# Performance work log

Measured on AMD Instinct MI355X. Metric: run time of the kernel, lower is better.

Reference implementation:

```python
import jax, jax.numpy as jnp
import numpy as np

OUT, IN, BLK, RANK = 4096, 4096, 32, 16
N_BLOCKS = IN // BLK  # 128
Q_ZERO = 128.0  # center of unsigned code range, maps codes to signed values


def setup_inputs() -> dict:
    key = jax.random.key(0)
    ks = jax.random.split(key, 6)
    x = jax.random.normal(ks[0], (4, 2048, IN), dtype=jnp.float32)
    # GGML-style block-quantized weight: int codes in blocks of 32 + per-block fp scale
    q_weight = jax.random.randint(ks[1], (OUT, N_BLOCKS, BLK), 0, 256, dtype=jnp.int32)
    scales = jax.random.uniform(ks[2], (OUT, N_BLOCKS), dtype=jnp.float32) * 0.02
    # LoRA patch applied to dequantized weight
    lora_up = jax.random.normal(ks[3], (OUT, RANK), dtype=jnp.float32) * 0.02
    lora_down = jax.random.normal(ks[4], (RANK, IN), dtype=jnp.float32) * 0.02
    bias = jax.random.normal(ks[5], (OUT,), dtype=jnp.float32)
    return {"x": x, "q_weight": q_weight, "scales": scales,
            "lora_up": lora_up, "lora_down": lora_down, "bias": bias}


def reference(x, q_weight, scales, lora_up, lora_down, bias):
    # 1) dequantize: per-block scale * centered int codes -> full fp weight [OUT, IN]
    w = (q_weight.astype(jnp.float32) - Q_ZERO) * scales[:, :, None]
    w = w.reshape(OUT, IN)
    # 2) apply LoRA patch to the dequantized weight (patch function in get_weight)
    w = w + lora_up @ lora_down
    # 3) delegate to the linear forward operation: y = x @ W^T + b
    return jnp.einsum('bsd,od->bso', x, w) + bias
```

## Files before the change

kernel.cpp:

```cpp
#include <hip/hip_runtime.h>
#include <cstdint>
#include <cstddef>

#define M_TOT 8192
#define N_TOT 4096
#define K_TOT 4096
#define RANK  16

#define BM 256
#define BN 256
#define BK 64
#define NT (K_TOT / BK)

typedef float f32x4 __attribute__((ext_vector_type(4)));
typedef __bf16 bf16x8 __attribute__((ext_vector_type(8)));
typedef unsigned short u16x8 __attribute__((ext_vector_type(8)));

__device__ __forceinline__ unsigned short f32_to_bf16(float f) {
    union { float f; uint32_t u; } v; v.f = f;
    uint32_t r = v.u + (0x7fffu + ((v.u >> 16) & 1u));
    return (unsigned short)(r >> 16);
}

__device__ __forceinline__ void gload_lds16(const void* g, void* l) {
    __builtin_amdgcn_global_load_lds(
        (const __attribute__((address_space(1))) void*)g,
        (__attribute__((address_space(3))) void*)l,
        16, 0, 0);
}

__global__ __launch_bounds__(256) void convert_x_kernel(const float* __restrict__ x,
                                                        unsigned short* __restrict__ xb,
                                                        int n8) {
    int i = blockIdx.x * 256 + threadIdx.x;
    if (i >= n8) return;
    float4 a = ((const float4*)x)[2 * (size_t)i];
    float4 b = ((const float4*)x)[2 * (size_t)i + 1];
    u16x8 o;
    o[0] = f32_to_bf16(a.x); o[1] = f32_to_bf16(a.y);
    o[2] = f32_to_bf16(a.z); o[3] = f32_to_bf16(a.w);
    o[4] = f32_to_bf16(b.x); o[5] = f32_to_bf16(b.y);
    o[6] = f32_to_bf16(b.z); o[7] = f32_to_bf16(b.w);
    *(u16x8*)&xb[(size_t)i * 8] = o;
}

__global__ __launch_bounds__(256) void build_w_kernel(const int* __restrict__ q,
                                                      const float* __restrict__ scales,
                                                      const float* __restrict__ up,
                                                      const float* __restrict__ down,
                                                      unsigned short* __restrict__ W) {
    const int o0 = blockIdx.x * 4;
    const int t = threadIdx.x;
    __shared__ float u[4][RANK];
    if (t < 64) u[t >> 4][t & 15] = up[(o0 + (t >> 4)) * RANK + (t & 15)];
    __syncthreads();

#pragma unroll
    for (int cc = 0; cc < 2; cc++) {
        const int c = t + 256 * cc;
        const int k0 = c * 8;
        float acc[4][8];
#pragma unroll
        for (int row = 0; row < 4; row++) {
            const int o = o0 + row;
            int4 qa = *(const int4*)&q[(size_t)o * K_TOT + k0];
            int4 qb = *(const int4*)&q[(size_t)o * K_TOT + k0 + 4];
            const float s = scales[o * (K_TOT / 32) + (k0 >> 5)];
            acc[row][0] = (float)(qa.x - 128) * s;
            acc[row][1] = (float)(qa.y - 128) * s;
            acc[row][2] = (float)(qa.z - 128) * s;
            acc[row][3] = (float)(qa.w - 128) * s;
            acc[row][4] = (float)(qb.x - 128) * s;
            acc[row][5] = (float)(qb.y - 128) * s;
            acc[row][6] = (float)(qb.z - 128) * s;
            acc[row][7] = (float)(qb.w - 128) * s;
        }
#pragma unroll
        for (int r = 0; r < RANK; r++) {
            float4 da = *(const float4*)&down[r * K_TOT + k0];
            float4 db = *(const float4*)&down[r * K_TOT + k0 + 4];
#pragma unroll
            for (int row = 0; row < 4; row++) {
                const float ur = u[row][r];
                acc[row][0] += ur * da.x; acc[row][1] += ur * da.y;
                acc[row][2] += ur * da.z; acc[row][3] += ur * da.w;
                acc[row][4] += ur * db.x; acc[row][5] += ur * db.y;
                acc[row][6] += ur * db.z; acc[row][7] += ur * db.w;
            }
        }
#pragma unroll
        for (int row = 0; row < 4; row++) {
            u16x8 o8;
#pragma unroll
            for (int j = 0; j < 8; j++) o8[j] = f32_to_bf16(acc[row][j]);
            *(u16x8*)&W[(size_t)(o0 + row) * K_TOT + k0] = o8;
        }
    }
}

#define BARRIER() do { asm volatile("" ::: "memory"); \
                       __builtin_amdgcn_s_barrier(); \
                       asm volatile("" ::: "memory"); } while (0)
#define WAITL0()  asm volatile("s_waitcnt lgkmcnt(0)" ::: "memory")
#define SCHED0()  __builtin_amdgcn_sched_barrier(0)

__global__ __launch_bounds__(512, 2) void gemm_bt_kernel(const unsigned short* __restrict__ A,
                                                         const unsigned short* __restrict__ B,
                                                         const float* __restrict__ bias,
                                                         float* __restrict__ C) {
    __shared__ unsigned short As[2][2][128 * BK];
    __shared__ unsigned short Bs[2][2][128 * BK];

    const int tid  = (int)threadIdx.x;
    const int wave = tid >> 6;
    const int lane = tid & 63;
    const int wm   = wave >> 2;
    const int wn   = wave & 3;
    const int wbh  = wn >> 1;
    const int wbr  = (wn & 1) * 64;

    int lin = (int)(blockIdx.y * gridDim.x + blockIdx.x);
    lin = (lin & 7) * 64 + (lin >> 3);
    const int tile_n = (lin & 15) * BN;
    const int tile_m = (lin >> 4) * BM;

    const int srow  = tid >> 3;
    const int sk    = ((tid & 7) ^ (srow & 7)) * 8;
    const int wbase = wave * 512;

    const int l16  = lane & 15;
    const int quad = lane >> 4;
    const int sw   = l16 & 7;
    const int slot0 = ((quad ^ sw) * 8);
    const int slot1 = (((4 + quad) ^ sw) * 8);

    const unsigned short* aBase = A + (size_t)(tile_m + srow) * K_TOT + sk;
    const unsigned short* bBase = B + (size_t)(tile_n + srow) * K_TOT + sk;

#define STAGE_A(d, h, t) do { \
    gload_lds16(aBase + (size_t)((h) * 128) * K_TOT + (size_t)(t) * BK, &As[d][h][wbase]); \
    gload_lds16(aBase + (size_t)((h) * 128 + 64) * K_TOT + (size_t)(t) * BK, &As[d][h][4096 + wbase]); \
  } while (0)
#define STAGE_B(d, h, t) do { \
    gload_lds16(bBase + (size_t)((h) * 128) * K_TOT + (size_t)(t) * BK, &Bs[d][h][wbase]); \
    gload_lds16(bBase + (size_t)((h) * 128 + 64) * K_TOT + (size_t)(t) * BK, &Bs[d][h][4096 + wbase]); \
  } while (0)

    f32x4 acc[8][4];
#pragma unroll
    for (int i = 0; i < 8; i++)
#pragma unroll
        for (int j = 0; j < 4; j++) { f32x4 z = {0.f, 0.f, 0.f, 0.f}; acc[i][j] = z; }

    STAGE_A(0, 0, 0); STAGE_A(0, 1, 0);
    STAGE_B(0, 0, 0); STAGE_B(0, 1, 0);
    STAGE_A(1, 0, 1); STAGE_A(1, 1, 1);
    asm volatile("s_waitcnt vmcnt(4)" ::: "memory");
    BARRIER();

    for (int t = 0; t < NT; ++t) {
        const int cur = t & 1, nxt = cur ^ 1;
        const unsigned short* __restrict__ Ah = &As[cur][wm][l16 * BK];
        const unsigned short* __restrict__ Bh = &Bs[cur][wbh][(wbr + l16) * BK];

        bf16x8 bA[4], bB[4], aF[4];

        if (t + 1 < NT) STAGE_B(nxt, 0, t + 1);
#pragma unroll
        for (int ni = 0; ni < 4; ni++) bA[ni] = *(const bf16x8*)&Bh[(ni * 16) * BK + slot0];
#pragma unroll
        for (int mi = 0; mi < 4; mi++) aF[mi] = *(const bf16x8*)&Ah[(mi * 16) * BK + slot0];
        BARRIER();
        WAITL0();
        SCHED0();
        __builtin_amdgcn_s_setprio(1);
#pragma unroll
        for (int mi = 0; mi < 4; mi++)
#pragma unroll
            for (int ni = 0; ni < 4; ni++)
                acc[mi][ni] = __builtin_amdgcn_mfma_f32_16x16x32_bf16(aF[mi], bA[ni], acc[mi][ni], 0, 0, 0);
        __builtin_amdgcn_s_setprio(0);
        SCHED0();
        BARRIER();

        if (t + 1 < NT) STAGE_B(nxt, 1, t + 1);
#pragma unroll
        for (int ni = 0; ni < 4; ni++) bB[ni] = *(const bf16x8*)&Bh[(ni * 16) * BK + slot1];
#pragma unroll
        for (int mi = 0; mi < 4; mi++) aF[mi] = *(const bf16x8*)&Ah[(mi * 16) * BK + slot1];
        BARRIER();
        WAITL0();
        SCHED0();
        __builtin_amdgcn_s_setprio(1);
#pragma unroll
        for (int mi = 0; mi < 4; mi++)
#pragma unroll
            for (int ni = 0; ni < 4; ni++)
                acc[mi][ni] = __builtin_amdgcn_mfma_f32_16x16x32_bf16(aF[mi], bB[ni], acc[mi][ni], 0, 0, 0);
        __builtin_amdgcn_s_setprio(0);
        SCHED0();
        BARRIER();

#pragma unroll
        for (int mi = 0; mi < 4; mi++) aF[mi] = *(const bf16x8*)&Ah[((mi + 4) * 16) * BK + slot0];
        BARRIER();
        WAITL0();
        SCHED0();
        __builtin_amdgcn_s_setprio(1);
#pragma unroll
        for (int mi = 0; mi < 4; mi++)
#pragma unroll
            for (int ni = 0; ni < 4; ni++)
                acc[mi + 4][ni] = __builtin_amdgcn_mfma_f32_16x16x32_bf16(aF[mi], bA[ni], acc[mi + 4][ni], 0, 0, 0);
        __builtin_amdgcn_s_setprio(0);
        SCHED0();
        BARRIER();

#pragma unroll
        for (int mi = 0; mi < 4; mi++) aF[mi] = *(const bf16x8*)&Ah[((mi + 4) * 16) * BK + slot1];
        BARRIER();
        if (t + 2 < NT) { STAGE_A(cur, 0, t + 2); STAGE_A(cur, 1, t + 2); }
        WAITL0();
        SCHED0();
        __builtin_amdgcn_s_setprio(1);
#pragma unroll
        for (int mi = 0; mi < 4; mi++)
#pragma unroll
            for (int ni = 0; ni < 4; ni++)
                acc[mi + 4][ni] = __builtin_amdgcn_mfma_f32_16x16x32_bf16(aF[mi], bB[ni], acc[mi + 4][ni], 0, 0, 0);
        __builtin_amdgcn_s_setprio(0);
        SCHED0();
        if (t + 1 < NT) {
            if (t + 2 < NT) asm volatile("s_waitcnt vmcnt(4)" ::: "memory");
            else            asm volatile("s_waitcnt vmcnt(0)" ::: "memory");
        }
        BARRIER();
    }

#pragma unroll
    for (int ni = 0; ni < 4; ni++) {
        const int col = tile_n + wn * 64 + ni * 16 + l16;
        const float bv = bias[col];
#pragma unroll
        for (int mi = 0; mi < 8; mi++) {
#pragma unroll
            for (int r = 0; r < 4; r++) {
                const int row = tile_m + wm * 128 + mi * 16 + quad * 4 + r;
                C[(size_t)row * N_TOT + col] = acc[mi][ni][r] + bv;
            }
        }
    }
#undef STAGE_A
#undef STAGE_B
}

extern "C" void kernel_launch(void* const* d_in, const int* in_sizes, int n_in,
                              void* d_out, int out_size, void* d_ws, size_t ws_size,
                              hipStream_t stream) {
    const float* x      = (const float*)d_in[0];
    const int*   q      = (const int*)d_in[1];
    const float* scales = (const float*)d_in[2];
    const float* up     = (const float*)d_in[3];
    const float* down   = (const float*)d_in[4];
    const float* bias   = (const float*)d_in[5];
    float* out = (float*)d_out;

    unsigned short* xb = (unsigned short*)d_ws;
    unsigned short* wb = xb + (size_t)M_TOT * K_TOT;

    const int n8 = M_TOT * K_TOT / 8;
    convert_x_kernel<<<n8 / 256, 256, 0, stream>>>(x, xb, n8);
    build_w_kernel<<<N_TOT / 4, 256, 0, stream>>>(q, scales, up, down, wb);
    gemm_bt_kernel<<<dim3(N_TOT / BN, M_TOT / BM), 512, 0, stream>>>(xb, wb, bias, out);
}
```

Measured before the change: 598.0 us.

## Restructure GEMM main loop with inline-asm LDS reads and one-tile-ahead A prefetch

The main loop of the bf16 GEMM now loads its LDS fragments through inline-asm ds_read_b128 on precomputed LDS addresses, and the global-to-LDS loads are issued after those reads. The A prefetch moves from two tiles ahead into the current buffer to one tile ahead into the next buffer, and every iteration ends with a full vmcnt(0) wait. The aim is cheaper address math and a simpler, more regular schedule. The cost is a shallower prefetch for A and a full drain of outstanding global loads each iteration, which can expose memory latency.

```diff
diff --git a/kernel.cpp b/kernel.cpp
--- a/kernel.cpp
+++ b/kernel.cpp
@@ -27,6 +27,16 @@
         (const __attribute__((address_space(1))) void*)g,
         (__attribute__((address_space(3))) void*)l,
         16, 0, 0);
+}
+
+__device__ __forceinline__ unsigned lds_addr(const void* p) {
+    return (unsigned)(uintptr_t)(const __attribute__((address_space(3))) void*)p;
+}
+
+__device__ __forceinline__ bf16x8 dsr(unsigned addr) {
+    bf16x8 r;
+    asm volatile("ds_read_b128 %0, %1" : "=v"(r) : "v"(addr));
+    return r;
 }
 
 __global__ __launch_bounds__(256) void convert_x_kernel(const float* __restrict__ x,
@@ -102,6 +112,7 @@
                        __builtin_amdgcn_s_barrier(); \
                        asm volatile("" ::: "memory"); } while (0)
 #define WAITL0()  asm volatile("s_waitcnt lgkmcnt(0)" ::: "memory")
+#define VMCNT0()  asm volatile("s_waitcnt vmcnt(0)" ::: "memory")
 #define SCHED0()  __builtin_amdgcn_sched_barrier(0)
 
 __global__ __launch_bounds__(512, 2) void gemm_bt_kernel(const unsigned short* __restrict__ A,
@@ -154,86 +165,85 @@
 
     STAGE_A(0, 0, 0); STAGE_A(0, 1, 0);
     STAGE_B(0, 0, 0); STAGE_B(0, 1, 0);
-    STAGE_A(1, 0, 1); STAGE_A(1, 1, 1);
-    asm volatile("s_waitcnt vmcnt(4)" ::: "memory");
+    VMCNT0();
     BARRIER();
 
     for (int t = 0; t < NT; ++t) {
         const int cur = t & 1, nxt = cur ^ 1;
-        const unsigned short* __restrict__ Ah = &As[cur][wm][l16 * BK];
-        const unsigned short* __restrict__ Bh = &Bs[cur][wbh][(wbr + l16) * BK];
-
-        bf16x8 bA[4], bB[4], aF[4];
-
+
+        const unsigned AhB = lds_addr(&As[cur][wm][l16 * BK]);
+        const unsigned BhB = lds_addr(&Bs[cur][wbh][(wbr + l16) * BK]);
+        const unsigned a0 = AhB + slot0 * 2, a1 = AhB + slot1 * 2;
+        const unsigned b0 = BhB + slot0 * 2, b1 = BhB + slot1 * 2;
+
+        bf16x8 bA[4], bB[4], aK[4];
+
+#pragma unroll
+        for (int ni = 0; ni < 4; ni++) bA[ni] = dsr(b0 + ni * 2048);
+#pragma unroll
+        for (int mi = 0; mi < 4; mi++) aK[mi] = dsr(a0 + mi * 2048);
         if (t + 1 < NT) STAGE_B(nxt, 0, t + 1);
-#pragma unroll
-        for (int ni = 0; ni < 4; ni++) bA[ni] = *(const bf16x8*)&Bh[(ni * 16) * BK + slot0];
-#pragma unroll
-        for (int mi = 0; mi < 4; mi++) aF[mi] = *(const bf16x8*)&Ah[(mi * 16) * BK + slot0];
-        BARRIER();
-        WAITL0();
-        SCHED0();
-        __builtin_amdgcn_s_setprio(1);
-#pragma unroll
-        for (int mi = 0; mi < 4; mi++)
-#pragma unroll
-            for (int ni = 0; ni < 4; ni++)
-                acc[mi][ni] = __builtin_amdgcn_mfma_f32_16x16x32_bf16(aF[mi], bA[ni], acc[mi][ni], 0, 0, 0);
-        __builtin_amdgcn_s_setprio(0);
-        SCHED0();
-        BARRIER();
-
+        BARRIER();
+        WAITL0();
+        SCHED0();
+        __builtin_amdgcn_s_setprio(1);
+#pragma unroll
+        for (int mi = 0; mi < 4; mi++)
+#pragma unroll
+            for (int ni = 0; ni < 4; ni++)
+                acc[mi][ni] = __builtin_amdgcn_mfma_f32_16x16x32_bf16(aK[mi], bA[ni], acc[mi][ni], 0, 0, 0);
+        __builtin_amdgcn_s_setprio(0);
+        SCHED0();
+        BARRIER();
+
+#pragma unroll
+        for (int ni = 0; ni < 4; ni++) bB[ni] = dsr(b1 + ni * 2048);
+#pragma unroll
+        for (int mi = 0; mi < 4; mi++) aK[mi] = dsr(a1 + mi * 2048);
         if (t + 1 < NT) STAGE_B(nxt, 1, t + 1);
-#pragma unroll
-        for (int ni = 0; ni < 4; ni++) bB[ni] = *(const bf16x8*)&Bh[(ni * 16) * BK + slot1];
-#pragma unroll
-        for (int mi = 0; mi < 4; mi++) aF[mi] = *(const bf16x8*)&Ah[(mi * 16) * BK + slot1];
-        BARRIER();
-        WAITL0();
-        SCHED0();
-        __builtin_amdgcn_s_setprio(1);
-#pragma unroll
-        for (int mi = 0; mi < 4; mi++)
-#pragma unroll
-            for (int ni = 0; ni < 4; ni++)
-                acc[mi][ni] = __builtin_amdgcn_mfma_f32_16x16x32_bf16(aF[mi], bB[ni], acc[mi][ni], 0, 0, 0);
-        __builtin_amdgcn_s_setprio(0);
-        SCHED0();
-        BARRIER();
-
-#pragma unroll
-        for (int mi = 0; mi < 4; mi++) aF[mi] = *(const bf16x8*)&Ah[((mi + 4) * 16) * BK + slot0];
-        BARRIER();
-        WAITL0();
-        SCHED0();
-        __builtin_amdgcn_s_setprio(1);
-#pragma unroll
-        for (int mi = 0; mi < 4; mi++)
-#pragma unroll
-            for (int ni = 0; ni < 4; ni++)
-                acc[mi + 4][ni] = __builtin_amdgcn_mfma_f32_16x16x32_bf16(aF[mi], bA[ni], acc[mi + 4][ni], 0, 0, 0);
-        __builtin_amdgcn_s_setprio(0);
-        SCHED0();
-        BARRIER();
-
-#pragma unroll
-        for (int mi = 0; mi < 4; mi++) aF[mi] = *(const bf16x8*)&Ah[((mi + 4) * 16) * BK + slot1];
-        BARRIER();
-        if (t + 2 < NT) { STAGE_A(cur, 0, t + 2); STAGE_A(cur, 1, t + 2); }
-        WAITL0();
-        SCHED0();
-        __builtin_amdgcn_s_setprio(1);
-#pragma unroll
-        for (int mi = 0; mi < 4; mi++)
-#pragma unroll
-            for (int ni = 0; ni < 4; ni++)
-                acc[mi + 4][ni] = __builtin_amdgcn_mfma_f32_16x16x32_bf16(aF[mi], bB[ni], acc[mi + 4][ni], 0, 0, 0);
-        __builtin_amdgcn_s_setprio(0);
-        SCHED0();
-        if (t + 1 < NT) {
-            if (t + 2 < NT) asm volatile("s_waitcnt vmcnt(4)" ::: "memory");
-            else            asm volatile("s_waitcnt vmcnt(0)" ::: "memory");
-        }
+        BARRIER();
+        WAITL0();
+        SCHED0();
+        __builtin_amdgcn_s_setprio(1);
+#pragma unroll
+        for (int mi = 0; mi < 4; mi++)
+#pragma unroll
+            for (int ni = 0; ni < 4; ni++)
+                acc[mi][ni] = __builtin_amdgcn_mfma_f32_16x16x32_bf16(aK[mi], bB[ni], acc[mi][ni], 0, 0, 0);
+        __builtin_amdgcn_s_setprio(0);
+        SCHED0();
+        BARRIER();
+
+#pragma unroll
+        for (int mi = 0; mi < 4; mi++) aK[mi] = dsr(a0 + 8192 + mi * 2048);
+        if (t + 1 < NT) { STAGE_A(nxt, 0, t + 1); STAGE_A(nxt, 1, t + 1); }
+        BARRIER();
+        WAITL0();
+        SCHED0();
+        __builtin_amdgcn_s_setprio(1);
+#pragma unroll
+        for (int mi = 0; mi < 4; mi++)
+#pragma unroll
+            for (int ni = 0; ni < 4; ni++)
+                acc[mi + 4][ni] = __builtin_amdgcn_mfma_f32_16x16x32_bf16(aK[mi], bA[ni], acc[mi + 4][ni], 0, 0, 0);
+        __builtin_amdgcn_s_setprio(0);
+        SCHED0();
+        BARRIER();
+
+#pragma unroll
+        for (int mi = 0; mi < 4; mi++) aK[mi] = dsr(a1 + 8192 + mi * 2048);
+        BARRIER();
+        WAITL0();
+        SCHED0();
+        __builtin_amdgcn_s_setprio(1);
+#pragma unroll
+        for (int mi = 0; mi < 4; mi++)
+#pragma unroll
+            for (int ni = 0; ni < 4; ni++)
+                acc[mi + 4][ni] = __builtin_amdgcn_mfma_f32_16x16x32_bf16(aK[mi], bB[ni], acc[mi + 4][ni], 0, 0, 0);
+        __builtin_amdgcn_s_setprio(0);
+        SCHED0();
+        VMCNT0();
         BARRIER();
     }
 
```

Result: faster. 542.4 us (-9.3%).
